# Performance work log

Measured on AMD Instinct MI355X. Metric: run time of the kernel, lower is better.

## Reference

```python
import jax, jax.numpy as jnp
import numpy as np

D_MODEL = 2048
NUM_HEADS = 16
D_FF = 8192
BATCH = 4
SEQ = 2048


def setup_inputs() -> dict:
    key = jax.random.key(0)
    ks = jax.random.split(key, 16)
    s_attn = 1.0 / np.sqrt(D_MODEL)
    s_ff1 = 1.0 / np.sqrt(D_MODEL)
    s_ff2 = 1.0 / np.sqrt(D_FF)
    return {
        "x": jax.random.normal(ks[0], (BATCH, SEQ, D_MODEL), dtype=jnp.float32),
        "Wq": jax.random.normal(ks[1], (D_MODEL, D_MODEL), dtype=jnp.float32) * s_attn,
        "bq": jnp.zeros((D_MODEL,), dtype=jnp.float32),
        "Wk": jax.random.normal(ks[2], (D_MODEL, D_MODEL), dtype=jnp.float32) * s_attn,
        "bk": jnp.zeros((D_MODEL,), dtype=jnp.float32),
        "Wv": jax.random.normal(ks[3], (D_MODEL, D_MODEL), dtype=jnp.float32) * s_attn,
        "bv": jnp.zeros((D_MODEL,), dtype=jnp.float32),
        "Wo": jax.random.normal(ks[4], (D_MODEL, D_MODEL), dtype=jnp.float32) * s_attn,
        "bo": jnp.zeros((D_MODEL,), dtype=jnp.float32),
        "W1": jax.random.normal(ks[5], (D_MODEL, D_FF), dtype=jnp.float32) * s_ff1,
        "b1": jnp.zeros((D_FF,), dtype=jnp.float32),
        "W2": jax.random.normal(ks[6], (D_FF, D_MODEL), dtype=jnp.float32) * s_ff2,
        "b2": jnp.zeros((D_MODEL,), dtype=jnp.float32),
        "ln1_g": jnp.ones((D_MODEL,), dtype=jnp.float32),
        "ln1_b": jnp.zeros((D_MODEL,), dtype=jnp.float32),
        "ln2_g": jnp.ones((D_MODEL,), dtype=jnp.float32),
        "ln2_b": jnp.zeros((D_MODEL,), dtype=jnp.float32),
    }


def _layer_norm(x, g, b, eps=1e-5):
    mu = jnp.mean(x, axis=-1, keepdims=True)
    var = jnp.mean(jnp.square(x - mu), axis=-1, keepdims=True)
    return (x - mu) * jax.lax.rsqrt(var + eps) * g + b


def _attention(h, Wq, bq, Wk, bk, Wv, bv, Wo, bo):
    B, S, D = h.shape
    H = NUM_HEADS
    dk = D // H
    q = (h @ Wq + bq).reshape(B, S, H, dk).transpose(0, 2, 1, 3)  # bhsd
    k = (h @ Wk + bk).reshape(B, S, H, dk).transpose(0, 2, 1, 3)
    v = (h @ Wv + bv).reshape(B, S, H, dk).transpose(0, 2, 1, 3)
    logits = jnp.einsum("bhqd,bhkd->bhqk", q, k) / jnp.sqrt(jnp.float32(dk))
    causal = jnp.triu(jnp.ones((S, S), dtype=bool), k=1)  # True above diagonal
    logits = jnp.where(causal, -jnp.inf, logits)
    attn = jax.nn.softmax(logits, axis=-1)
    out = jnp.einsum("bhqk,bhkd->bhqd", attn, v)
    out = out.transpose(0, 2, 1, 3).reshape(B, S, D)
    return out @ Wo + bo


def reference(x, Wq, bq, Wk, bk, Wv, bv, Wo, bo, W1, b1, W2, b2,
              ln1_g, ln1_b, ln2_g, ln2_b):
    # Pre-LN attention block + residual
    h = _layer_norm(x, ln1_g, ln1_b)
    x = x + _attention(h, Wq, bq, Wk, bk, Wv, bv, Wo, bo)
    # Pre-LN FFN block + residual (GELU activation)
    h = _layer_norm(x, ln2_g, ln2_b)
    ff = jax.nn.gelu(h @ W1 + b1, approximate=False) @ W2 + b2
    return x + ff
```

## Files before the change

### kernel.cpp

```cpp
#include <hip/hip_runtime.h>
#include <hip/hip_bf16.h>

#define D_MODEL 2048
#define NUM_HEADS 16
#define D_FF 8192
#define BATCH 4
#define SEQ 2048
#define DK 128
#define MTOT (BATCH * SEQ)

typedef __attribute__((ext_vector_type(8))) short short8;
typedef __attribute__((ext_vector_type(4))) short short4v;
typedef __attribute__((ext_vector_type(4))) float f32x4;

#define MFMA16(a, b, c) __builtin_amdgcn_mfma_f32_16x16x32_bf16(a, b, c, 0, 0, 0)

#define GLOAD16(gp, lp)                                                        \
  __builtin_amdgcn_global_load_lds(                                            \
      (const __attribute__((address_space(1))) void*)(gp),                     \
      (__attribute__((address_space(3))) void*)(lp), 16, 0, 0)

static __device__ __forceinline__ unsigned short f2bf(float f) {
  return __builtin_bit_cast(unsigned short, __float2bfloat16(f));
}

__global__ __launch_bounds__(256) void transpose_cvt_kernel(
    const float* __restrict__ in, __hip_bfloat16* __restrict__ out, int K, int N) {
  __shared__ float tile[32][33];
  const int n0 = blockIdx.x * 32, k0 = blockIdx.y * 32;
  const int tx = threadIdx.x & 31, ty = threadIdx.x >> 5;
#pragma unroll
  for (int i = 0; i < 4; ++i)
    tile[ty + i * 8][tx] = in[(size_t)(k0 + ty + i * 8) * N + n0 + tx];
  __syncthreads();
#pragma unroll
  for (int i = 0; i < 4; ++i)
    out[(size_t)(n0 + ty + i * 8) * K + k0 + tx] = __float2bfloat16(tile[tx][ty + i * 8]);
}

__global__ __launch_bounds__(256) void layernorm_kernel(
    const float* __restrict__ x, const float* __restrict__ g,
    const float* __restrict__ bta, __hip_bfloat16* __restrict__ out) {
  const int row = blockIdx.x;
  const int tid = threadIdx.x;
  const float* xr = x + (size_t)row * D_MODEL;
  float4 v0 = *(const float4*)(xr + tid * 8);
  float4 v1 = *(const float4*)(xr + tid * 8 + 4);
  float s = v0.x + v0.y + v0.z + v0.w + v1.x + v1.y + v1.z + v1.w;
  float q = v0.x * v0.x + v0.y * v0.y + v0.z * v0.z + v0.w * v0.w +
            v1.x * v1.x + v1.y * v1.y + v1.z * v1.z + v1.w * v1.w;
#pragma unroll
  for (int off = 1; off < 64; off <<= 1) {
    s += __shfl_xor(s, off);
    q += __shfl_xor(q, off);
  }
  __shared__ float rs[4], rq[4];
  if ((tid & 63) == 0) {
    rs[tid >> 6] = s;
    rq[tid >> 6] = q;
  }
  __syncthreads();
  s = rs[0] + rs[1] + rs[2] + rs[3];
  q = rq[0] + rq[1] + rq[2] + rq[3];
  const float mu = s * (1.0f / D_MODEL);
  const float var = q * (1.0f / D_MODEL) - mu * mu;
  const float rstd = rsqrtf(var + 1e-5f);
  float4 g0 = *(const float4*)(g + tid * 8);
  float4 g1 = *(const float4*)(g + tid * 8 + 4);
  float4 b0 = *(const float4*)(bta + tid * 8);
  float4 b1 = *(const float4*)(bta + tid * 8 + 4);
  short8 o;
  o[0] = (short)f2bf((v0.x - mu) * rstd * g0.x + b0.x);
  o[1] = (short)f2bf((v0.y - mu) * rstd * g0.y + b0.y);
  o[2] = (short)f2bf((v0.z - mu) * rstd * g0.z + b0.z);
  o[3] = (short)f2bf((v0.w - mu) * rstd * g0.w + b0.w);
  o[4] = (short)f2bf((v1.x - mu) * rstd * g1.x + b1.x);
  o[5] = (short)f2bf((v1.y - mu) * rstd * g1.y + b1.y);
  o[6] = (short)f2bf((v1.z - mu) * rstd * g1.z + b1.z);
  o[7] = (short)f2bf((v1.w - mu) * rstd * g1.w + b1.w);
  *(short8*)(out + (size_t)row * D_MODEL + tid * 8) = o;
}

enum { EPI_BF16 = 0, EPI_VT = 1, EPI_RESID = 2, EPI_GELU = 3 };

#define AF_MFMA_PHASE(FI0)                                                     \
  {                                                                            \
    const int raA = wm + (FI0) * 16 + l15;                                     \
    const int raB = wm + ((FI0) + 1) * 16 + l15;                               \
    short8 aA0 = *(const short8*)(db + raA * 128 + ((lg ^ (raA & 7)) << 4));   \
    short8 aB0 = *(const short8*)(db + raB * 128 + ((lg ^ (raB & 7)) << 4));   \
    short8 aA1 =                                                               \
        *(const short8*)(db + raA * 128 + (((4 + lg) ^ (raA & 7)) << 4));      \
    short8 aB1 =                                                               \
        *(const short8*)(db + raB * 128 + (((4 + lg) ^ (raB & 7)) << 4));      \
    __builtin_amdgcn_s_barrier();                                              \
    asm volatile("s_waitcnt lgkmcnt(0)" ::: "memory");                         \
    __builtin_amdgcn_sched_barrier(0);                                         \
    __builtin_amdgcn_s_setprio(1);                                             \
    _Pragma("unroll") for (int fj = 0; fj < 4; ++fj)                           \
        acc[FI0][fj] = MFMA16(aA0, bf0[fj], acc[FI0][fj]);                     \
    _Pragma("unroll") for (int fj = 0; fj < 4; ++fj)                           \
        acc[(FI0) + 1][fj] = MFMA16(aB0, bf0[fj], acc[(FI0) + 1][fj]);         \
    _Pragma("unroll") for (int fj = 0; fj < 4; ++fj)                           \
        acc[FI0][fj] = MFMA16(aA1, bf1[fj], acc[FI0][fj]);                     \
    _Pragma("unroll") for (int fj = 0; fj < 4; ++fj)                           \
        acc[(FI0) + 1][fj] = MFMA16(aB1, bf1[fj], acc[(FI0) + 1][fj]);         \
    __builtin_amdgcn_s_setprio(0);                                             \
  }

template <int EPI>
__global__ __launch_bounds__(512, 2) void gemm_kernel(
    const __hip_bfloat16* __restrict__ A, const __hip_bfloat16* __restrict__ Bt,
    const float* __restrict__ bias, const float* __restrict__ resid,
    void* __restrict__ outv, int M, int N, int K) {
  __shared__ __align__(16) unsigned char lds[2][65536];
  const int tid = threadIdx.x;
  const int lane = tid & 63, w = tid >> 6;
  const int l15 = lane & 15, lg = lane >> 4;
  const int d = blockIdx.x;
  const int x = d & 7;
  const int i = d >> 3;
  const int cC = (i & 7) + 8 * (i >> 5);
  const int rC = x + 8 * ((i >> 3) & 3);
  const int m0 = rC * 256, n0 = cC * 256;
  const int wm = (w >> 2) * 128, wn = (w & 3) * 64;

  f32x4 acc[8][4] = {};

  const int row8 = lane >> 3;
  const int g8 = (lane & 7) ^ row8;
  const int wa = (w & 3) + ((w >> 2) * 16);

  auto stA = [&](int tt, int c) {
    GLOAD16(A + (size_t)(m0 + c * 8 + row8) * K + (size_t)tt * 64 + g8 * 8,
            lds[tt & 1] + c * 1024);
  };
  auto stB = [&](int tt, int c) {
    GLOAD16(Bt + (size_t)(n0 + c * 8 + row8) * K + (size_t)tt * 64 + g8 * 8,
            lds[tt & 1] + 32768 + c * 1024);
  };

  const int nt = K >> 6;

  stB(0, w); stB(0, 8 + w); stA(0, wa);
  stB(0, 16 + w); stB(0, 24 + w); stA(0, wa + 4);
  stA(0, wa + 8); stA(0, wa + 12);
  stB(1, w); stB(1, 8 + w); stA(1, wa);
  stB(1, 16 + w); stB(1, 24 + w); stA(1, wa + 4);
  stA(1, wa + 8);
  asm volatile("s_waitcnt vmcnt(7)" ::: "memory");
  __builtin_amdgcn_s_barrier();

  for (int t = 0; t < nt; ++t) {
    const unsigned char* db = lds[t & 1];
    const bool s1 = (t + 1 < nt), s2 = (t + 2 < nt);
    short8 bf0[4], bf1[4];
    if (s1) stA(t + 1, wa + 12);
#pragma unroll
    for (int f = 0; f < 4; ++f) {
      const int rb = wn + f * 16 + l15;
      bf0[f] = *(const short8*)(db + 32768 + rb * 128 + ((lg ^ (rb & 7)) << 4));
      bf1[f] =
          *(const short8*)(db + 32768 + rb * 128 + (((4 + lg) ^ (rb & 7)) << 4));
    }
    AF_MFMA_PHASE(0)
    __builtin_amdgcn_s_barrier();
    if (s2) { stB(t + 2, w); stB(t + 2, 8 + w); stA(t + 2, wa); }
    AF_MFMA_PHASE(2)
    __builtin_amdgcn_s_barrier();
    if (s2) { stB(t + 2, 16 + w); stB(t + 2, 24 + w); stA(t + 2, wa + 4); }
    AF_MFMA_PHASE(4)
    __builtin_amdgcn_s_barrier();
    if (s2) stA(t + 2, wa + 8);
    AF_MFMA_PHASE(6)
    if (s2)
      asm volatile("s_waitcnt vmcnt(7)" ::: "memory");
    else
      asm volatile("s_waitcnt vmcnt(0)" ::: "memory");
    __builtin_amdgcn_s_barrier();
  }

#pragma unroll
  for (int fi = 0; fi < 8; ++fi) {
#pragma unroll
    for (int fj = 0; fj < 4; ++fj) {
      const int mb = m0 + wm + fi * 16 + lg * 4;
      const int n = n0 + wn + fj * 16 + l15;
      const float bv = bias ? bias[n] : 0.0f;
      if constexpr (EPI == EPI_VT) {
        const int bb = mb >> 11, ss = mb & (SEQ - 1);
        const int hh = n >> 7, dd = n & (DK - 1);
        short4v pk;
#pragma unroll
        for (int r = 0; r < 4; ++r) pk[r] = (short)f2bf(acc[fi][fj][r] + bv);
        __hip_bfloat16* o = (__hip_bfloat16*)outv;
        *(short4v*)(o + ((size_t)((bb * NUM_HEADS + hh) * DK + dd)) * SEQ + ss) = pk;
      } else {
#pragma unroll
        for (int r = 0; r < 4; ++r) {
          const int m = mb + r;
          const float v = acc[fi][fj][r] + bv;
          if constexpr (EPI == EPI_BF16) {
            ((__hip_bfloat16*)outv)[(size_t)m * N + n] = __float2bfloat16(v);
          } else if constexpr (EPI == EPI_GELU) {
            const float ge = 0.5f * v * (1.0f + erff(v * 0.70710678118654752f));
            ((__hip_bfloat16*)outv)[(size_t)m * N + n] = __float2bfloat16(ge);
          } else {
            ((float*)outv)[(size_t)m * N + n] = resid[(size_t)m * N + n] + v;
          }
        }
      }
    }
  }
}

__global__ __launch_bounds__(512, 4) void attn_kernel(
    const __hip_bfloat16* __restrict__ Qm, const __hip_bfloat16* __restrict__ Km,
    const __hip_bfloat16* __restrict__ Vt, __hip_bfloat16* __restrict__ Om) {
  __shared__ __align__(16) unsigned char Kl[2][16384];
  __shared__ __align__(16) unsigned char Vl[2][16384];
  __shared__ __align__(16) unsigned char Pl[16384];
  const int tid = threadIdx.x;
  const int lane = tid & 63, w = tid >> 6;
  const int l15 = lane & 15, lg = lane >> 4;
  const int bh = blockIdx.y, b = bh >> 4, h = bh & 15;
  const int q0 = ((int)gridDim.x - 1 - (int)blockIdx.x) * 128;
  const int qw = q0 + w * 16;
  const int row8 = lane >> 3;
  const int nt = (q0 >> 6) + 2;

  short8 qf[4];
  const __hip_bfloat16* qbase = Qm + (size_t)(b * SEQ + qw + l15) * D_MODEL + h * DK;
#pragma unroll
  for (int ks = 0; ks < 4; ++ks) qf[ks] = *(const short8*)(qbase + ks * 32 + lg * 8);

  float m_run[4], l_run[4];
  f32x4 acc_o[8];
#pragma unroll
  for (int r = 0; r < 4; ++r) { m_run[r] = -1e30f; l_run[r] = 0.0f; }
#pragma unroll
  for (int fd = 0; fd < 8; ++fd) acc_o[fd] = (f32x4){0.f, 0.f, 0.f, 0.f};

  auto STAGE = [&](int tt) {
    unsigned char* kb = Kl[tt & 1];
    unsigned char* vb = Vl[tt & 1];
    const int t0 = tt * 64;
#pragma unroll
    for (int i = 0; i < 2; ++i) {
      const int c = w * 2 + i;
      const int row = c * 4 + lg;
      const int gcb = l15 ^ (row & 7);
      GLOAD16(Km + (size_t)(b * SEQ + t0 + row) * D_MODEL + h * DK + gcb * 8,
              kb + c * 1024);
    }
#pragma unroll
    for (int i = 0; i < 2; ++i) {
      const int c = w * 2 + i;
      const int row = c * 8 + row8;
      const int gcb = (lane & 7) ^ (row & 7);
      GLOAD16(Vt + (size_t)(bh * DK + row) * SEQ + t0 + gcb * 8, vb + c * 1024);
    }
  };

  STAGE(0);
  for (int t = 0; t < nt; ++t) {
    const int t0 = t * 64;
    if (t + 1 < nt) {
      STAGE(t + 1);
      asm volatile("s_waitcnt vmcnt(4)" ::: "memory");
    } else {
      asm volatile("s_waitcnt vmcnt(0)" ::: "memory");
    }
    __builtin_amdgcn_s_barrier();
    asm volatile("" ::: "memory");
    if (t0 <= qw + 15) {
      const unsigned char* kb = Kl[t & 1];
      const unsigned char* vb = Vl[t & 1];
      f32x4 sacc[4];
#pragma unroll
      for (int fn = 0; fn < 4; ++fn) sacc[fn] = (f32x4){0.f, 0.f, 0.f, 0.f};
      __builtin_amdgcn_s_setprio(1);
#pragma unroll
      for (int ks = 0; ks < 4; ++ks) {
        const int cb = ks * 4 + lg;
#pragma unroll
        for (int fn = 0; fn < 4; ++fn) {
          const int rn = fn * 16 + l15;
          short8 kf = *(const short8*)(kb + rn * 256 + ((cb ^ (rn & 7)) << 4));
          sacc[fn] = MFMA16(qf[ks], kf, sacc[fn]);
        }
      }
      __builtin_amdgcn_s_setprio(0);
      const float scale = 0.088388347648318447f;
      float mt[4] = {-1e30f, -1e30f, -1e30f, -1e30f};
#pragma unroll
      for (int fn = 0; fn < 4; ++fn) {
        const int key = t0 + fn * 16 + l15;
#pragma unroll
        for (int r = 0; r < 4; ++r) {
          const int qg = qw + lg * 4 + r;
          float sv = sacc[fn][r] * scale;
          sv = (key <= qg) ? sv : -1e30f;
          sacc[fn][r] = sv;
          mt[r] = fmaxf(mt[r], sv);
        }
      }
#pragma unroll
      for (int r = 0; r < 4; ++r)
#pragma unroll
        for (int off = 1; off < 16; off <<= 1) mt[r] = fmaxf(mt[r], __shfl_xor(mt[r], off));
      int ok = 1;
#pragma unroll
      for (int r = 0; r < 4; ++r) ok = ok && (mt[r] <= m_run[r] + 8.0f);
      const bool defer = __all(ok);
      float alpha[4];
      if (!defer) {
#pragma unroll
        for (int r = 0; r < 4; ++r) {
          const float mnew = fmaxf(m_run[r], mt[r]);
          alpha[r] = __expf(m_run[r] - mnew);
          m_run[r] = mnew;
        }
      }
      float ls[4] = {0.f, 0.f, 0.f, 0.f};
#pragma unroll
      for (int fn = 0; fn < 4; ++fn)
#pragma unroll
        for (int r = 0; r < 4; ++r) {
          const float p = __expf(sacc[fn][r] - m_run[r]);
          sacc[fn][r] = p;
          ls[r] += p;
        }
#pragma unroll
      for (int r = 0; r < 4; ++r) {
#pragma unroll
        for (int off = 1; off < 16; off <<= 1) ls[r] += __shfl_xor(ls[r], off);
        l_run[r] = (defer ? l_run[r] : l_run[r] * alpha[r]) + ls[r];
      }
      if (!defer) {
#pragma unroll
        for (int fd = 0; fd < 8; ++fd)
#pragma unroll
          for (int r = 0; r < 4; ++r) acc_o[fd][r] *= alpha[r];
      }
      unsigned char* pw = Pl + w * 2048;
#pragma unroll
      for (int fn = 0; fn < 4; ++fn) {
        const int tt = fn * 16 + l15;
#pragma unroll
        for (int r = 0; r < 4; ++r) {
          const int qq = lg * 4 + r;
          *(unsigned short*)(pw + qq * 128 +
                             ((((tt >> 3) + qq + (qq >> 3)) & 7) << 4) +
                             (tt & 7) * 2) = f2bf(sacc[fn][r]);
        }
      }
#pragma unroll
      for (int ks = 0; ks < 2; ++ks) {
        const int tb = ks * 4 + lg;
        short8 pf = *(const short8*)(Pl + w * 2048 + l15 * 128 +
                                     (((tb + l15 + (l15 >> 3)) & 7) << 4));
        const int cb = ks * 4 + lg;
        __builtin_amdgcn_s_setprio(1);
#pragma unroll
        for (int fd = 0; fd < 8; ++fd) {
          const int rv = fd * 16 + l15;
          short8 vf = *(const short8*)(vb + rv * 128 + ((cb ^ (rv & 7)) << 4));
          acc_o[fd] = MFMA16(pf, vf, acc_o[fd]);
        }
        __builtin_amdgcn_s_setprio(0);
      }
    }
    asm volatile("" ::: "memory");
    __builtin_amdgcn_s_barrier();
    asm volatile("" ::: "memory");
  }
#pragma unroll
  for (int r = 0; r < 4; ++r) {
    const float inv = 1.0f / l_run[r];
    const int qg = qw + lg * 4 + r;
    __hip_bfloat16* ob = Om + (size_t)(b * SEQ + qg) * D_MODEL + h * DK + l15;
#pragma unroll
    for (int fd = 0; fd < 8; ++fd)
      ob[fd * 16] = __float2bfloat16(acc_o[fd][r] * inv);
  }
}

extern "C" void kernel_launch(void* const* d_in, const int* in_sizes, int n_in,
                              void* d_out, int out_size, void* d_ws, size_t ws_size,
                              hipStream_t stream) {
  (void)in_sizes; (void)n_in; (void)out_size;
  const size_t MB = 1024 * 1024;
  if (ws_size < 192 * MB) return;

  const float* x  = (const float*)d_in[0];
  const float* Wq = (const float*)d_in[1];
  const float* bq = (const float*)d_in[2];
  const float* Wk = (const float*)d_in[3];
  const float* bk = (const float*)d_in[4];
  const float* Wv = (const float*)d_in[5];
  const float* bv = (const float*)d_in[6];
  const float* Wo = (const float*)d_in[7];
  const float* bo = (const float*)d_in[8];
  const float* W1 = (const float*)d_in[9];
  const float* b1 = (const float*)d_in[10];
  const float* W2 = (const float*)d_in[11];
  const float* b2 = (const float*)d_in[12];
  const float* g1 = (const float*)d_in[13];
  const float* be1 = (const float*)d_in[14];
  const float* g2 = (const float*)d_in[15];
  const float* be2 = (const float*)d_in[16];

  char* ws = (char*)d_ws;
  __hip_bfloat16* Hb  = (__hip_bfloat16*)(ws + 0 * MB);
  __hip_bfloat16* Qb  = (__hip_bfloat16*)(ws + 32 * MB);
  __hip_bfloat16* Kb  = (__hip_bfloat16*)(ws + 64 * MB);
  __hip_bfloat16* Vtb = (__hip_bfloat16*)(ws + 96 * MB);
  __hip_bfloat16* AOb = (__hip_bfloat16*)(ws + 128 * MB);
  __hip_bfloat16* FF1 = (__hip_bfloat16*)(ws + 32 * MB);
  __hip_bfloat16* WqT = (__hip_bfloat16*)(ws + 160 * MB);
  __hip_bfloat16* WkT = (__hip_bfloat16*)(ws + 168 * MB);
  __hip_bfloat16* WvT = (__hip_bfloat16*)(ws + 176 * MB);
  __hip_bfloat16* WoT = (__hip_bfloat16*)(ws + 184 * MB);
  __hip_bfloat16* W1T = (__hip_bfloat16*)(ws + 160 * MB);
  __hip_bfloat16* W2T = (__hip_bfloat16*)(ws + 160 * MB);
  float* X2 = (float*)d_out;

  const dim3 tb(256);
  transpose_cvt_kernel<<<dim3(64, 64), tb, 0, stream>>>(Wq, WqT, 2048, 2048);
  transpose_cvt_kernel<<<dim3(64, 64), tb, 0, stream>>>(Wk, WkT, 2048, 2048);
  transpose_cvt_kernel<<<dim3(64, 64), tb, 0, stream>>>(Wv, WvT, 2048, 2048);
  transpose_cvt_kernel<<<dim3(64, 64), tb, 0, stream>>>(Wo, WoT, 2048, 2048);

  layernorm_kernel<<<MTOT, tb, 0, stream>>>(x, g1, be1, Hb);

  gemm_kernel<EPI_BF16><<<256, 512, 0, stream>>>(Hb, WqT, bq, nullptr, Qb, MTOT, 2048, 2048);
  gemm_kernel<EPI_BF16><<<256, 512, 0, stream>>>(Hb, WkT, bk, nullptr, Kb, MTOT, 2048, 2048);
  gemm_kernel<EPI_VT><<<256, 512, 0, stream>>>(Hb, WvT, bv, nullptr, Vtb, MTOT, 2048, 2048);

  attn_kernel<<<dim3(SEQ / 128, BATCH * NUM_HEADS), dim3(512), 0, stream>>>(Qb, Kb, Vtb, AOb);

  gemm_kernel<EPI_RESID><<<256, 512, 0, stream>>>(AOb, WoT, bo, x, X2, MTOT, 2048, 2048);

  layernorm_kernel<<<MTOT, tb, 0, stream>>>(X2, g2, be2, Hb);

  transpose_cvt_kernel<<<dim3(256, 64), tb, 0, stream>>>(W1, W1T, 2048, 8192);
  gemm_kernel<EPI_GELU><<<1024, 512, 0, stream>>>(Hb, W1T, b1, nullptr, FF1, MTOT, 8192, 2048);
  transpose_cvt_kernel<<<dim3(64, 256), tb, 0, stream>>>(W2, W2T, 8192, 2048);
  gemm_kernel<EPI_RESID><<<256, 512, 0, stream>>>(FF1, W2T, b2, X2, X2, MTOT, 2048, 8192);
}
```

Before: 1.226 ms.

## Compute transposed scores so P stays in registers, dropping LDS round-trip

The QK^T MFMA operands are swapped so each lane holds one query row's scores. Row max and row sum then need only two cross-lane shuffles instead of sixteen per row. The probability tile is repacked into the PV operand layout with register shuffles instead of being written to and read back from shared memory, which removes the P LDS buffer. In exchange it adds many __shfl operations per tile, plus broadcasts of alpha and l back to the accumulator layout.

```diff
diff --git a/kernel.cpp b/kernel.cpp
--- a/kernel.cpp
+++ b/kernel.cpp
@@ -219,7 +219,6 @@
     const __hip_bfloat16* __restrict__ Vt, __hip_bfloat16* __restrict__ Om) {
   __shared__ __align__(16) unsigned char Kl[2][16384];
   __shared__ __align__(16) unsigned char Vl[2][16384];
-  __shared__ __align__(16) unsigned char Pl[16384];
   const int tid = threadIdx.x;
   const int lane = tid & 63, w = tid >> 6;
   const int l15 = lane & 15, lg = lane >> 4;
@@ -234,23 +233,21 @@
 #pragma unroll
   for (int ks = 0; ks < 4; ++ks) qf[ks] = *(const short8*)(qbase + ks * 32 + lg * 8);
 
-  float m_run[4], l_run[4];
+  float m_run = -1e30f, l_run = 0.0f;
   f32x4 acc_o[8];
-#pragma unroll
-  for (int r = 0; r < 4; ++r) { m_run[r] = -1e30f; l_run[r] = 0.0f; }
 #pragma unroll
   for (int fd = 0; fd < 8; ++fd) acc_o[fd] = (f32x4){0.f, 0.f, 0.f, 0.f};
 
   auto STAGE = [&](int tt) {
     unsigned char* kb = Kl[tt & 1];
     unsigned char* vb = Vl[tt & 1];
-    const int t0 = tt * 64;
+    const int t0s = tt * 64;
 #pragma unroll
     for (int i = 0; i < 2; ++i) {
       const int c = w * 2 + i;
       const int row = c * 4 + lg;
       const int gcb = l15 ^ (row & 7);
-      GLOAD16(Km + (size_t)(b * SEQ + t0 + row) * D_MODEL + h * DK + gcb * 8,
+      GLOAD16(Km + (size_t)(b * SEQ + t0s + row) * D_MODEL + h * DK + gcb * 8,
               kb + c * 1024);
     }
 #pragma unroll
@@ -258,7 +255,7 @@
       const int c = w * 2 + i;
       const int row = c * 8 + row8;
       const int gcb = (lane & 7) ^ (row & 7);
-      GLOAD16(Vt + (size_t)(bh * DK + row) * SEQ + t0 + gcb * 8, vb + c * 1024);
+      GLOAD16(Vt + (size_t)(bh * DK + row) * SEQ + t0s + gcb * 8, vb + c * 1024);
     }
   };
 
@@ -287,80 +284,70 @@
         for (int fn = 0; fn < 4; ++fn) {
           const int rn = fn * 16 + l15;
           short8 kf = *(const short8*)(kb + rn * 256 + ((cb ^ (rn & 7)) << 4));
-          sacc[fn] = MFMA16(qf[ks], kf, sacc[fn]);
+          sacc[fn] = MFMA16(kf, qf[ks], sacc[fn]);
         }
       }
       __builtin_amdgcn_s_setprio(0);
       const float scale = 0.088388347648318447f;
-      float mt[4] = {-1e30f, -1e30f, -1e30f, -1e30f};
+      const int qg = qw + l15;
+      float mt = -1e30f;
 #pragma unroll
       for (int fn = 0; fn < 4; ++fn) {
-        const int key = t0 + fn * 16 + l15;
+        const int keyb = t0 + fn * 16 + lg * 4;
 #pragma unroll
         for (int r = 0; r < 4; ++r) {
-          const int qg = qw + lg * 4 + r;
           float sv = sacc[fn][r] * scale;
-          sv = (key <= qg) ? sv : -1e30f;
+          sv = (keyb + r <= qg) ? sv : -1e30f;
           sacc[fn][r] = sv;
-          mt[r] = fmaxf(mt[r], sv);
-        }
-      }
-#pragma unroll
-      for (int r = 0; r < 4; ++r)
-#pragma unroll
-        for (int off = 1; off < 16; off <<= 1) mt[r] = fmaxf(mt[r], __shfl_xor(mt[r], off));
-      int ok = 1;
-#pragma unroll
-      for (int r = 0; r < 4; ++r) ok = ok && (mt[r] <= m_run[r] + 8.0f);
-      const bool defer = __all(ok);
-      float alpha[4];
+          mt = fmaxf(mt, sv);
+        }
+      }
+      mt = fmaxf(mt, __shfl_xor(mt, 16));
+      mt = fmaxf(mt, __shfl_xor(mt, 32));
+      const bool defer = __all(mt <= m_run + 8.0f);
+      float alpha = 1.0f;
       if (!defer) {
+        const float mnew = fmaxf(m_run, mt);
+        alpha = __expf(m_run - mnew);
+        m_run = mnew;
+      }
+      float ls = 0.0f;
+#pragma unroll
+      for (int fn = 0; fn < 4; ++fn)
 #pragma unroll
         for (int r = 0; r < 4; ++r) {
-          const float mnew = fmaxf(m_run[r], mt[r]);
-          alpha[r] = __expf(m_run[r] - mnew);
-          m_run[r] = mnew;
-        }
-      }
-      float ls[4] = {0.f, 0.f, 0.f, 0.f};
-#pragma unroll
-      for (int fn = 0; fn < 4; ++fn)
-#pragma unroll
-        for (int r = 0; r < 4; ++r) {
-          const float p = __expf(sacc[fn][r] - m_run[r]);
+          const float p = __expf(sacc[fn][r] - m_run);
           sacc[fn][r] = p;
-          ls[r] += p;
-        }
-#pragma unroll
-      for (int r = 0; r < 4; ++r) {
-#pragma unroll
-        for (int off = 1; off < 16; off <<= 1) ls[r] += __shfl_xor(ls[r], off);
-        l_run[r] = (defer ? l_run[r] : l_run[r] * alpha[r]) + ls[r];
-      }
+          ls += p;
+        }
+      ls += __shfl_xor(ls, 16);
+      ls += __shfl_xor(ls, 32);
+      l_run = (defer ? l_run : l_run * alpha) + ls;
       if (!defer) {
+        float abr[4];
+#pragma unroll
+        for (int r = 0; r < 4; ++r) abr[r] = __shfl(alpha, lg * 4 + r);
 #pragma unroll
         for (int fd = 0; fd < 8; ++fd)
 #pragma unroll
-          for (int r = 0; r < 4; ++r) acc_o[fd][r] *= alpha[r];
-      }
-      unsigned char* pw = Pl + w * 2048;
-#pragma unroll
-      for (int fn = 0; fn < 4; ++fn) {
-        const int tt = fn * 16 + l15;
-#pragma unroll
-        for (int r = 0; r < 4; ++r) {
-          const int qq = lg * 4 + r;
-          *(unsigned short*)(pw + qq * 128 +
-                             ((((tt >> 3) + qq + (qq >> 3)) & 7) << 4) +
-                             (tt & 7) * 2) = f2bf(sacc[fn][r]);
-        }
-      }
-#pragma unroll
-      for (int ks = 0; ks < 2; ++ks) {
-        const int tb = ks * 4 + lg;
-        short8 pf = *(const short8*)(Pl + w * 2048 + l15 * 128 +
-                                     (((tb + l15 + (l15 >> 3)) & 7) << 4));
-        const int cb = ks * 4 + lg;
+          for (int r = 0; r < 4; ++r) acc_o[fd][r] *= abr[r];
+      }
+      const int srcLo = l15 + 16 * (2 * (lg & 1));
+      const int srcHi = srcLo + 16;
+      const int hi = lg >> 1;
+#pragma unroll
+      for (int s = 0; s < 2; ++s) {
+        short8 pf;
+#pragma unroll
+        for (int j = 0; j < 4; ++j) {
+          const float v0 = __shfl(sacc[2 * s][j], srcLo);
+          const float v1 = __shfl(sacc[2 * s + 1][j], srcLo);
+          pf[j] = (short)f2bf(hi ? v1 : v0);
+          const float w0 = __shfl(sacc[2 * s][j], srcHi);
+          const float w1 = __shfl(sacc[2 * s + 1][j], srcHi);
+          pf[4 + j] = (short)f2bf(hi ? w1 : w0);
+        }
+        const int cb = s * 4 + lg;
         __builtin_amdgcn_s_setprio(1);
 #pragma unroll
         for (int fd = 0; fd < 8; ++fd) {
@@ -375,9 +362,12 @@
     __builtin_amdgcn_s_barrier();
     asm volatile("" ::: "memory");
   }
+  float linv[4];
+#pragma unroll
+  for (int r = 0; r < 4; ++r) linv[r] = __shfl(l_run, lg * 4 + r);
 #pragma unroll
   for (int r = 0; r < 4; ++r) {
-    const float inv = 1.0f / l_run[r];
+    const float inv = 1.0f / linv[r];
     const int qg = qw + lg * 4 + r;
     __hip_bfloat16* ob = Om + (size_t)(b * SEQ + qg) * D_MODEL + h * DK + l15;
 #pragma unroll
```

New measurement: 1.190 ms. 2.9% less time.
